# Optimization experiments

Hardware: AMD Instinct MI355X
Metric: run time of the kernel (lower is better)

Reference implementation:

```python
import jax, jax.numpy as jnp
import numpy as np

B = 8192       # batch (tokens)
D = 2048       # data_dim
DEPTH = 3      # tree depth: 1 root + 2 mid + 4 leaf experts
INIT = 0.02


def setup_inputs() -> dict:
    key = jax.random.key(0)
    ks = jax.random.split(key, 6)
    x = jax.random.normal(ks[0], (B, D), dtype=jnp.float32)
    # router output simulated as i.i.d. path bits (router is a frozen pretrained black box)
    path_mask = jax.random.randint(ks[1], (B, DEPTH), 0, 2, dtype=jnp.int32)
    W0 = jax.random.normal(ks[2], (D, D), dtype=jnp.float32) * INIT
    b0 = jnp.zeros((D,), dtype=jnp.float32)
    W1 = jax.random.normal(ks[3], (2, D, D), dtype=jnp.float32) * INIT  # depth-1 experts
    b1 = jnp.zeros((2, D), dtype=jnp.float32)
    W2 = jax.random.normal(ks[4], (4, D, D), dtype=jnp.float32) * INIT  # depth-2 (leaf) experts
    b2 = jnp.zeros((4, D), dtype=jnp.float32)
    return {"x": x, "W0": W0, "b0": b0, "W1": W1, "b1": b1,
            "W2": W2, "b2": b2, "path_mask": path_mask}


def reference(x, W0, b0, W1, b1, W2, b2, path_mask):
    # Root expert (depth 0): applied to all tokens.
    h0 = jax.nn.relu(x @ W0 + b0)                                  # [B, D]
    bit0 = path_mask[:, 0]                                          # routes depth-1 children
    bit1 = path_mask[:, 1]                                          # routes depth-2 children
    # Depth-1: 2 experts; dense compute then per-token select (static-shape MoE dispatch).
    h1_all = jax.nn.relu(jnp.einsum('bd,edf->bef', h0, W1) + b1)    # [B, 2, D]
    h1 = jnp.take_along_axis(h1_all, bit0[:, None, None].astype(jnp.int32), axis=1)[:, 0]
    # Depth-2 (leaves): 4 experts indexed by the 2-bit path.
    leaf = 2 * bit0 + bit1                                          # [B] in {0,1,2,3}
    h2_all = jax.nn.relu(jnp.einsum('bd,edf->bef', h1, W2) + b2)    # [B, 4, D]
    y = jnp.take_along_axis(h2_all, leaf[:, None, None].astype(jnp.int32), axis=1)[:, 0]
    return y
```

## Files before the change

### kernel.cpp

```cpp
#include <hip/hip_runtime.h>

#define BB 8192
#define DD 2048
#define NSLOT 7
#define NP1 (BB + 2*256)
#define NP2 (BB + 4*256)

typedef unsigned short u16;
typedef unsigned int   u32;
typedef unsigned long long u64;

typedef __bf16 bf16x8 __attribute__((ext_vector_type(8)));
typedef float  f32x4  __attribute__((ext_vector_type(4)));
typedef u16    u16x8  __attribute__((ext_vector_type(8)));

#define OFF_WT   0ull
#define OFF_XB   (OFF_WT + (size_t)NSLOT*DD*DD*2)
#define OFF_H0   (OFF_XB + (size_t)BB*DD*2)
#define OFF_P1   (OFF_H0 + (size_t)BB*DD*2)
#define OFF_P2   (OFF_P1 + (size_t)NP1*4)
#define OFF_META (OFF_P2 + (size_t)NP2*4)

__device__ __forceinline__ u16 f2bf(float f) {
  u32 u = __float_as_uint(f);
  u32 r = (u + 0x7FFFu + ((u >> 16) & 1u)) >> 16;
  return (u16)r;
}
__device__ __forceinline__ float bf2f(u16 u) {
  return __uint_as_float(((u32)u) << 16);
}

__device__ __forceinline__ void gld16(const void* g, void* l) {
  __builtin_amdgcn_global_load_lds(
      (const __attribute__((address_space(1))) void*)g,
      (__attribute__((address_space(3))) void*)l, 16, 0, 0);
}


__global__ void k_detect(const u16* x, int* meta) {
  __shared__ int cnt, cntz;
  if (threadIdx.x == 0) { cnt = 0; cntz = 0; }
  __syncthreads();
  u16 u = x[threadIdx.x * 17];
  int ex = (u >> 7) & 0xFF;
  int sane = (ex == 0) || (ex >= 112 && ex <= 143);
  atomicAdd(&cnt, sane);
  atomicAdd(&cntz, (u == 0) ? 1 : 0);
  __syncthreads();
  if (threadIdx.x == 0) meta[20] = (cnt >= 205 && cntz < 64) ? 1 : 0;
}

__global__ __launch_bounds__(1024) void k_route(const int* __restrict__ pm,
                                                int* __restrict__ p1,
                                                int* __restrict__ p2,
                                                int* __restrict__ meta) {
  __shared__ int cnt[6];
  __shared__ int cur[6];
  __shared__ int base1[2], base2[4];
  const int tid = threadIdx.x;
  const int lane = tid & 63;
  if (tid < 6) { cnt[tid] = 0; cur[tid] = 0; }
  __syncthreads();

  for (int i = tid; i < NP1; i += 1024) p1[i] = -1;
  for (int i = tid; i < NP2; i += 1024) p2[i] = -1;

  int myb0[8], myleaf[8];
  #pragma unroll
  for (int i = 0; i < 8; ++i) {
    int b = i * 1024 + tid;
    int b0 = pm[b*3] & 1, b1 = pm[b*3+1] & 1;
    myb0[i] = b0; myleaf[i] = b0*2 + b1;
  }
  #pragma unroll
  for (int i = 0; i < 8; ++i) {
    u64 m0 = __ballot(myb0[i] == 0);
    if (lane == 0) {
      atomicAdd(&cnt[0], __popcll(m0));
      atomicAdd(&cnt[1], 64 - __popcll(m0));
    }
    #pragma unroll
    for (int e = 0; e < 4; ++e) {
      u64 me = __ballot(myleaf[i] == e);
      if (lane == 0) atomicAdd(&cnt[2+e], __popcll(me));
    }
  }
  __syncthreads();
  if (tid == 0) {
    base1[0] = 0;
    base1[1] = (cnt[0] + 255) & ~255;
    meta[12] = 0; meta[13] = base1[1];
    meta[14] = base1[1] + ((cnt[1] + 255) & ~255);
    int b = 0;
    #pragma unroll
    for (int e = 0; e < 4; ++e) {
      base2[e] = b; meta[15+e] = b;
      b += (cnt[2+e] + 255) & ~255;
    }
    meta[19] = b;
  }
  __syncthreads();
  #pragma unroll
  for (int i = 0; i < 8; ++i) {
    int b = i * 1024 + tid;
    u64 lt = (1ull << lane) - 1ull;
    #pragma unroll
    for (int g = 0; g < 2; ++g) {
      u64 m = __ballot(myb0[i] == g);
      int pos = __popcll(m & lt);
      int wbase = 0;
      if (lane == 0 && m) wbase = atomicAdd(&cur[g], __popcll(m));
      wbase = __shfl(wbase, 0);
      if (myb0[i] == g) p1[base1[g] + wbase + pos] = b;
    }
    #pragma unroll
    for (int g = 0; g < 4; ++g) {
      u64 m = __ballot(myleaf[i] == g);
      int pos = __popcll(m & lt);
      int wbase = 0;
      if (lane == 0 && m) wbase = atomicAdd(&cur[2+g], __popcll(m));
      wbase = __shfl(wbase, 0);
      if (myleaf[i] == g) p2[base2[g] + wbase + pos] = b;
    }
  }
}

__global__ void k_cvtx(const void* __restrict__ x, u16* __restrict__ xb,
                       const int* __restrict__ meta) {
  int i = blockIdx.x * 256 + threadIdx.x;
  if (meta[20]) {
    ((uint4*)xb)[i] = ((const uint4*)x)[i];
  } else {
    const float4* p = (const float4*)x + (size_t)i * 2;
    float4 a = p[0], b = p[1];
    uint4 o;
    o.x = f2bf(a.x) | ((u32)f2bf(a.y) << 16);
    o.y = f2bf(a.z) | ((u32)f2bf(a.w) << 16);
    o.z = f2bf(b.x) | ((u32)f2bf(b.y) << 16);
    o.w = f2bf(b.z) | ((u32)f2bf(b.w) << 16);
    ((uint4*)xb)[i] = o;
  }
}

__global__ void k_wt(const void* __restrict__ W0, const void* __restrict__ W1,
                     const void* __restrict__ W2, u16* __restrict__ wt,
                     const int* __restrict__ meta) {
  __shared__ u16 tile[64][66];
  int bid = blockIdx.x;
  int slot = bid >> 10;
  int t = bid & 1023;
  int tr = t >> 5, tc = t & 31;
  const void* src; size_t eoff;
  if (slot == 0)      { src = W0; eoff = 0; }
  else if (slot <= 2) { src = W1; eoff = (size_t)(slot-1)*DD*DD; }
  else                { src = W2; eoff = (size_t)(slot-3)*DD*DD; }
  int r0 = tr*64, c0 = tc*64;
  int tid = threadIdx.x;
  int isbf = meta[20];
  #pragma unroll
  for (int i = 0; i < 4; ++i) {
    int idx = tid + i*256;
    int r = idx >> 4, c4 = (idx & 15) * 4;
    size_t goff = eoff + (size_t)(r0 + r)*DD + c0 + c4;
    u16 v0, v1, v2, v3;
    if (isbf) {
      ushort4 v = *(const ushort4*)((const u16*)src + goff);
      v0 = v.x; v1 = v.y; v2 = v.z; v3 = v.w;
    } else {
      float4 v = *(const float4*)((const float*)src + goff);
      v0 = f2bf(v.x); v1 = f2bf(v.y); v2 = f2bf(v.z); v3 = f2bf(v.w);
    }
    tile[r][c4+0] = v0; tile[r][c4+1] = v1;
    tile[r][c4+2] = v2; tile[r][c4+3] = v3;
  }
  __syncthreads();
  u16* dst = wt + (size_t)slot*DD*DD;
  #pragma unroll
  for (int i = 0; i < 2; ++i) {
    int idx = tid + i*256;
    int n = idx >> 3, j = idx & 7;
    u16x8 o;
    #pragma unroll
    for (int k = 0; k < 8; ++k) o[k] = tile[j*8 + k][n];
    *(u16x8*)&dst[(size_t)(c0 + n)*DD + r0 + j*8] = o;
  }
}

#define SBA(T) ((u32)(((T) & 3) * 24576))
#define SBB(T) ((u32)(((T) & 3) * 24576 + 16384))

#define TILE(T, STAGE, VMN) do {                                             \
  asm volatile("s_waitcnt vmcnt(" #VMN ")" ::: "memory");                    \
  __builtin_amdgcn_s_barrier();                                              \
  {                                                                          \
    if (STAGE) {                                                             \
      const int t3 = (T) + 3;                                                \
      gld16(gA0 + (size_t)t3 * 32, sm + SBA(t3) + wid * 1024);               \
      gld16(gA1 + (size_t)t3 * 32, sm + SBA(t3) + 8192 + wid * 1024);        \
      gld16(gB0 + (size_t)t3 * 32, sm + SBB(t3) + wid * 1024);               \
    }                                                                        \
    const u32 sa = SBA(T) + aoff;                                            \
    const u32 sb = SBB(T) + boff;                                            \
    bf16x8 af[4], bfr[4];                                                    \
    _Pragma("unroll") for (int mt = 0; mt < 4; ++mt)                         \
      af[mt] = *(const bf16x8*)(sm + sa + mt * 1024);                        \
    _Pragma("unroll") for (int nt = 0; nt < 4; ++nt)                         \
      bfr[nt] = *(const bf16x8*)(sm + sb + nt * 1024);                       \
    asm volatile("s_waitcnt lgkmcnt(0)" ::: "memory");                       \
    __builtin_amdgcn_sched_barrier(0);                                       \
    __builtin_amdgcn_s_setprio(1);                                           \
    _Pragma("unroll") for (int mt = 0; mt < 4; ++mt)                         \
      _Pragma("unroll") for (int nt = 0; nt < 4; ++nt)                       \
        acc[mt][nt] = __builtin_amdgcn_mfma_f32_16x16x32_bf16(               \
            af[mt], bfr[nt], acc[mt][nt], 0, 0, 0);                          \
    __builtin_amdgcn_s_setprio(0);                                           \
    __builtin_amdgcn_s_barrier();                                            \
  }                                                                          \
} while (0)

__global__ __launch_bounds__(512, 2) void k_gemm(
    const u16* __restrict__ A, const u16* __restrict__ Wt,
    const void* __restrict__ bias, const int* __restrict__ perm,
    const int* __restrict__ bases, int nexp,
    void* __restrict__ Out, int final_out, const int* __restrict__ meta) {
  __shared__ __align__(16) char sm[4 * 24576];

  const int tid  = threadIdx.x;
  const int wid  = tid >> 6;
  const int lane = tid & 63;

  const u32 nwg = gridDim.x * gridDim.y;
  const u32 wg  = blockIdx.y * gridDim.x + blockIdx.x;
  const u32 cpx = nwg >> 3;
  const u32 swz = (wg & 7u) * cpx + (wg >> 3);
  const int m0 = (int)(swz >> 4) * 256;
  const int n0 = (int)(swz & 15u) * 128;

  int e = 0;
  if (nexp == 2)      e = (m0 >= bases[1]);
  else if (nexp == 4) e = (m0 >= bases[1]) + (m0 >= bases[2]) + (m0 >= bases[3]);
  if (perm && m0 >= bases[nexp]) return;
  const u16* W = Wt + (size_t)e * DD * DD;

  const int sr = wid * 16 + (lane >> 2);
  const int kc = (lane & 3) * 8;
  int ar0 = m0 + sr, ar1 = m0 + 128 + sr;
  if (perm) {
    int v0 = perm[ar0]; ar0 = v0 < 0 ? 0 : v0;
    int v1 = perm[ar1]; ar1 = v1 < 0 ? 0 : v1;
  }
  const u16* gA0 = A + (size_t)ar0 * DD + kc;
  const u16* gA1 = A + (size_t)ar1 * DD + kc;
  const u16* gB0 = W + (size_t)(n0 + sr) * DD + kc;

  const int wm = wid >> 1, wn = wid & 1;
  const int q = lane >> 4, cl = lane & 15;
  const u32 aoff = (u32)((wm * 64 + cl) * 64 + q * 16);
  const u32 boff = (u32)((wn * 64 + cl) * 64 + q * 16);

  f32x4 zero = {0.0f, 0.0f, 0.0f, 0.0f};
  f32x4 acc[4][4];
  #pragma unroll
  for (int i = 0; i < 4; ++i)
    #pragma unroll
    for (int j = 0; j < 4; ++j) acc[i][j] = zero;

  #pragma unroll
  for (int tt = 0; tt < 3; ++tt) {
    gld16(gA0 + (size_t)tt * 32, sm + SBA(tt) + wid * 1024);
    gld16(gA1 + (size_t)tt * 32, sm + SBA(tt) + 8192 + wid * 1024);
    gld16(gB0 + (size_t)tt * 32, sm + SBB(tt) + wid * 1024);
  }

  #pragma unroll 1
  for (int t = 0; t < 61; ++t) TILE(t, true, 6);
  TILE(61, false, 6);
  TILE(62, false, 3);
  TILE(63, false, 0);

  const int isbf = meta[20];
  float bv[4];
  #pragma unroll
  for (int nt = 0; nt < 4; ++nt) {
    int col = n0 + wn * 64 + nt * 16 + cl;
    bv[nt] = isbf ? bf2f(((const u16*)bias)[e * DD + col])
                  : ((const float*)bias)[e * DD + col];
  }
  #pragma unroll
  for (int mt = 0; mt < 4; ++mt) {
    int rbase = m0 + wm * 64 + mt * 16 + q * 4;
    #pragma unroll
    for (int r = 0; r < 4; ++r) {
      int row = rbase + r;
      int orow = row;
      if (perm) { orow = perm[row]; if (orow < 0) continue; }
      #pragma unroll
      for (int nt = 0; nt < 4; ++nt) {
        int col = n0 + wn * 64 + nt * 16 + cl;
        float v = acc[mt][nt][r] + bv[nt];
        v = v > 0.0f ? v : 0.0f;
        if (!final_out || isbf) ((u16*)Out)[(size_t)orow * DD + col] = f2bf(v);
        else                    ((float*)Out)[(size_t)orow * DD + col] = v;
      }
    }
  }
}

#undef TILE
#undef SBA
#undef SBB

extern "C" void kernel_launch(void* const* d_in, const int* in_sizes, int n_in,
                              void* d_out, int out_size, void* d_ws, size_t ws_size,
                              hipStream_t stream) {
  (void)in_sizes; (void)n_in; (void)out_size; (void)ws_size;
  const void* x  = d_in[0];
  const void* W0 = d_in[1];
  const void* b0 = d_in[2];
  const void* W1 = d_in[3];
  const void* b1 = d_in[4];
  const void* W2 = d_in[5];
  const void* b2 = d_in[6];
  const int*  pm = (const int*)d_in[7];

  char* ws  = (char*)d_ws;
  u16*  wt  = (u16*)(ws + OFF_WT);
  u16*  xb  = (u16*)(ws + OFF_XB);
  u16*  h0  = (u16*)(ws + OFF_H0);
  u16*  h1  = xb;
  int*  p1  = (int*)(ws + OFF_P1);
  int*  p2  = (int*)(ws + OFF_P2);
  int*  meta= (int*)(ws + OFF_META);

  hipLaunchKernelGGL(k_detect, dim3(1),  dim3(256),  0, stream, (const u16*)x, meta);
  hipLaunchKernelGGL(k_route,  dim3(1),  dim3(1024), 0, stream, pm, p1, p2, meta);
  hipLaunchKernelGGL(k_cvtx,   dim3(BB*DD/8/256), dim3(256), 0, stream, x, xb, meta);
  hipLaunchKernelGGL(k_wt,     dim3(7*1024), dim3(256), 0, stream, W0, W1, W2, wt, meta);

  hipLaunchKernelGGL(k_gemm, dim3(16, 32), dim3(512), 0, stream,
                     xb, wt, b0, (const int*)nullptr, (const int*)nullptr, 1,
                     (void*)h0, 0, meta);
  hipLaunchKernelGGL(k_gemm, dim3(16, NP1/256), dim3(512), 0, stream,
                     h0, wt + (size_t)1*DD*DD, b1, p1, meta + 12, 2,
                     (void*)h1, 0, meta);
  hipLaunchKernelGGL(k_gemm, dim3(16, NP2/256), dim3(512), 0, stream,
                     h1, wt + (size_t)3*DD*DD, b2, p2, meta + 15, 4,
                     d_out, 1, meta);
}
```

Before: 558.2 us.

## Use 4-wave blocks with 128x64 warp tiles, 3-stage LDS pipeline, swizzled LDS

Cuts the GEMM block from 8 waves to 4 waves. Each wave now computes a 128x64 sub-tile with 32 accumulators, which raises register-level reuse of the A and B fragments. The LDS ring drops from 4 to 3 buffers, prefetching 2 tiles ahead, and uses an XOR swizzle on the k-chunk to avoid bank conflicts. The trade-off is higher register pressure per wave and less latency hiding, since there are fewer waves and a shallower prefetch.

```diff
diff --git a/kernel.cpp b/kernel.cpp
--- a/kernel.cpp
+++ b/kernel.cpp
@@ -186,30 +186,32 @@
   }
 }
 
-#define SBA(T) ((u32)(((T) & 3) * 24576))
-#define SBB(T) ((u32)(((T) & 3) * 24576 + 16384))
-
-#define TILE(T, STAGE, VMN) do {                                             \
+#define STG(SBUF, TI) do {                                                   \
+    const size_t ko = (size_t)(TI) * 32;                                     \
+    gld16(gA0 + ko, sm + (SBUF)*24576 +         0 + widoff);                 \
+    gld16(gA1 + ko, sm + (SBUF)*24576 +      4096 + widoff);                 \
+    gld16(gA2 + ko, sm + (SBUF)*24576 +      8192 + widoff);                 \
+    gld16(gA3 + ko, sm + (SBUF)*24576 +     12288 + widoff);                 \
+    gld16(gB0 + ko, sm + (SBUF)*24576 + 16384 + 0 + widoff);                 \
+    gld16(gB1 + ko, sm + (SBUF)*24576 + 16384 + 4096 + widoff);              \
+  } while (0)
+
+#define TILE(BUF, T, STAGE, SBUF, VMN) do {                                  \
   asm volatile("s_waitcnt vmcnt(" #VMN ")" ::: "memory");                    \
   __builtin_amdgcn_s_barrier();                                              \
   {                                                                          \
-    if (STAGE) {                                                             \
-      const int t3 = (T) + 3;                                                \
-      gld16(gA0 + (size_t)t3 * 32, sm + SBA(t3) + wid * 1024);               \
-      gld16(gA1 + (size_t)t3 * 32, sm + SBA(t3) + 8192 + wid * 1024);        \
-      gld16(gB0 + (size_t)t3 * 32, sm + SBB(t3) + wid * 1024);               \
-    }                                                                        \
-    const u32 sa = SBA(T) + aoff;                                            \
-    const u32 sb = SBB(T) + boff;                                            \
-    bf16x8 af[4], bfr[4];                                                    \
-    _Pragma("unroll") for (int mt = 0; mt < 4; ++mt)                         \
+    if (STAGE) STG(SBUF, (T) + 2);                                           \
+    const u32 sa = (BUF)*24576 + aoff;                                       \
+    const u32 sb = (BUF)*24576 + 16384 + boff;                               \
+    bf16x8 af[8], bfr[4];                                                    \
+    _Pragma("unroll") for (int mt = 0; mt < 8; ++mt)                         \
       af[mt] = *(const bf16x8*)(sm + sa + mt * 1024);                        \
     _Pragma("unroll") for (int nt = 0; nt < 4; ++nt)                         \
       bfr[nt] = *(const bf16x8*)(sm + sb + nt * 1024);                       \
     asm volatile("s_waitcnt lgkmcnt(0)" ::: "memory");                       \
     __builtin_amdgcn_sched_barrier(0);                                       \
     __builtin_amdgcn_s_setprio(1);                                           \
-    _Pragma("unroll") for (int mt = 0; mt < 4; ++mt)                         \
+    _Pragma("unroll") for (int mt = 0; mt < 8; ++mt)                         \
       _Pragma("unroll") for (int nt = 0; nt < 4; ++nt)                       \
         acc[mt][nt] = __builtin_amdgcn_mfma_f32_16x16x32_bf16(               \
             af[mt], bfr[nt], acc[mt][nt], 0, 0, 0);                          \
@@ -218,16 +220,17 @@
   }                                                                          \
 } while (0)
 
-__global__ __launch_bounds__(512, 2) void k_gemm(
+__global__ __launch_bounds__(256, 2) void k_gemm(
     const u16* __restrict__ A, const u16* __restrict__ Wt,
     const void* __restrict__ bias, const int* __restrict__ perm,
     const int* __restrict__ bases, int nexp,
     void* __restrict__ Out, int final_out, const int* __restrict__ meta) {
-  __shared__ __align__(16) char sm[4 * 24576];
+  __shared__ __align__(16) char sm[3 * 24576];
 
   const int tid  = threadIdx.x;
   const int wid  = tid >> 6;
   const int lane = tid & 63;
+  const u32 widoff = (u32)wid * 1024;
 
   const u32 nwg = gridDim.x * gridDim.y;
   const u32 wg  = blockIdx.y * gridDim.x + blockIdx.x;
@@ -242,41 +245,48 @@
   if (perm && m0 >= bases[nexp]) return;
   const u16* W = Wt + (size_t)e * DD * DD;
 
-  const int sr = wid * 16 + (lane >> 2);
-  const int kc = (lane & 3) * 8;
-  int ar0 = m0 + sr, ar1 = m0 + 128 + sr;
-  if (perm) {
-    int v0 = perm[ar0]; ar0 = v0 < 0 ? 0 : v0;
-    int v1 = perm[ar1]; ar1 = v1 < 0 ? 0 : v1;
-  }
-  const u16* gA0 = A + (size_t)ar0 * DD + kc;
-  const u16* gA1 = A + (size_t)ar1 * DD + kc;
+  const int sr = tid >> 2;
+  const int kc = ((tid & 3) ^ ((tid >> 3) & 3)) * 8;
+  int ar[4];
+  #pragma unroll
+  for (int j = 0; j < 4; ++j) {
+    int r = m0 + j * 64 + sr;
+    if (perm) { int v = perm[r]; r = (v < 0) ? 0 : v; }
+    ar[j] = r;
+  }
+  const u16* gA0 = A + (size_t)ar[0] * DD + kc;
+  const u16* gA1 = A + (size_t)ar[1] * DD + kc;
+  const u16* gA2 = A + (size_t)ar[2] * DD + kc;
+  const u16* gA3 = A + (size_t)ar[3] * DD + kc;
   const u16* gB0 = W + (size_t)(n0 + sr) * DD + kc;
+  const u16* gB1 = W + (size_t)(n0 + 64 + sr) * DD + kc;
 
   const int wm = wid >> 1, wn = wid & 1;
   const int q = lane >> 4, cl = lane & 15;
-  const u32 aoff = (u32)((wm * 64 + cl) * 64 + q * 16);
-  const u32 boff = (u32)((wn * 64 + cl) * 64 + q * 16);
+  const int sw = q ^ ((cl >> 1) & 3);
+  const u32 aoff = (u32)((wm * 128 + cl) * 64 + sw * 16);
+  const u32 boff = (u32)((wn * 64 + cl) * 64 + sw * 16);
 
   f32x4 zero = {0.0f, 0.0f, 0.0f, 0.0f};
-  f32x4 acc[4][4];
-  #pragma unroll
-  for (int i = 0; i < 4; ++i)
+  f32x4 acc[8][4];
+  #pragma unroll
+  for (int i = 0; i < 8; ++i)
     #pragma unroll
     for (int j = 0; j < 4; ++j) acc[i][j] = zero;
 
-  #pragma unroll
-  for (int tt = 0; tt < 3; ++tt) {
-    gld16(gA0 + (size_t)tt * 32, sm + SBA(tt) + wid * 1024);
-    gld16(gA1 + (size_t)tt * 32, sm + SBA(tt) + 8192 + wid * 1024);
-    gld16(gB0 + (size_t)tt * 32, sm + SBB(tt) + wid * 1024);
-  }
+  STG(0, 0);
+  STG(1, 1);
 
   #pragma unroll 1
-  for (int t = 0; t < 61; ++t) TILE(t, true, 6);
-  TILE(61, false, 6);
-  TILE(62, false, 3);
-  TILE(63, false, 0);
+  for (int t = 0; t < 60; t += 3) {
+    TILE(0, t + 0, 1, 2, 6);
+    TILE(1, t + 1, 1, 0, 6);
+    TILE(2, t + 2, 1, 1, 6);
+  }
+  TILE(0, 60, 1, 2, 6);
+  TILE(1, 61, 1, 0, 6);
+  TILE(2, 62, 0, 0, 6);
+  TILE(0, 63, 0, 0, 0);
 
   const int isbf = meta[20];
   float bv[4];
@@ -287,8 +297,8 @@
                   : ((const float*)bias)[e * DD + col];
   }
   #pragma unroll
-  for (int mt = 0; mt < 4; ++mt) {
-    int rbase = m0 + wm * 64 + mt * 16 + q * 4;
+  for (int mt = 0; mt < 8; ++mt) {
+    int rbase = m0 + wm * 128 + mt * 16 + q * 4;
     #pragma unroll
     for (int r = 0; r < 4; ++r) {
       int row = rbase + r;
@@ -307,8 +317,7 @@
 }
 
 #undef TILE
-#undef SBA
-#undef SBB
+#undef STG
 
 extern "C" void kernel_launch(void* const* d_in, const int* in_sizes, int n_in,
                               void* d_out, int out_size, void* d_ws, size_t ws_size,
@@ -337,13 +346,13 @@
   hipLaunchKernelGGL(k_cvtx,   dim3(BB*DD/8/256), dim3(256), 0, stream, x, xb, meta);
   hipLaunchKernelGGL(k_wt,     dim3(7*1024), dim3(256), 0, stream, W0, W1, W2, wt, meta);
 
-  hipLaunchKernelGGL(k_gemm, dim3(16, 32), dim3(512), 0, stream,
+  hipLaunchKernelGGL(k_gemm, dim3(16, 32), dim3(256), 0, stream,
                      xb, wt, b0, (const int*)nullptr, (const int*)nullptr, 1,
                      (void*)h0, 0, meta);
-  hipLaunchKernelGGL(k_gemm, dim3(16, NP1/256), dim3(512), 0, stream,
+  hipLaunchKernelGGL(k_gemm, dim3(16, NP1/256), dim3(256), 0, stream,
                      h0, wt + (size_t)1*DD*DD, b1, p1, meta + 12, 2,
                      (void*)h1, 0, meta);
-  hipLaunchKernelGGL(k_gemm, dim3(16, NP2/256), dim3(512), 0, stream,
+  hipLaunchKernelGGL(k_gemm, dim3(16, NP2/256), dim3(256), 0, stream,
                      h1, wt + (size_t)3*DD*DD, b2, p2, meta + 15, 4,
                      d_out, 1, meta);
 }
```

After: 522.5 us. -6.4%, faster.

## Restage GEMM mainloop with 64-wide K tiles, swizzled LDS and split half-stages

Applied to the files above, without the earlier changes.

The bf16 GEMM main loop now works on 64-wide K tiles. Each tile is split into two half-stages whose global-to-LDS loads are issued between the MFMA batches. The buffer ring grows to six 24KB LDS slots allocated dynamically. An XOR swizzle on the K-chunk column is meant to cut LDS bank conflicts, and the trailing per-tile barrier is removed. The goal is to hide more load latency and lower synchronisation cost per unit of K. In exchange, the roughly 147KB of LDS allows only one workgroup per CU, contrary to the launch-bounds hint, and relies on the device allowing that much dynamic LDS.

```diff
diff --git a/kernel.cpp b/kernel.cpp
--- a/kernel.cpp
+++ b/kernel.cpp
@@ -186,35 +186,47 @@
   }
 }
 
-#define SBA(T) ((u32)(((T) & 3) * 24576))
-#define SBB(T) ((u32)(((T) & 3) * 24576 + 16384))
-
-#define TILE(T, STAGE, VMN) do {                                             \
+#define STGH(SLOT, P, TI) do {                                               \
+    const size_t ko = (size_t)(TI) * 64;                                     \
+    gld16(gA##P##0 + ko, sm + (SLOT)*24576 +     0 + widoff);                \
+    gld16(gA##P##1 + ko, sm + (SLOT)*24576 +  8192 + widoff);                \
+    gld16(gB##P    + ko, sm + (SLOT)*24576 + 16384 + widoff);                \
+  } while (0)
+
+#define TILE(S0, S1, SS0, SS1, T, STAGE, VMN) do {                           \
   asm volatile("s_waitcnt vmcnt(" #VMN ")" ::: "memory");                    \
   __builtin_amdgcn_s_barrier();                                              \
   {                                                                          \
-    if (STAGE) {                                                             \
-      const int t3 = (T) + 3;                                                \
-      gld16(gA0 + (size_t)t3 * 32, sm + SBA(t3) + wid * 1024);               \
-      gld16(gA1 + (size_t)t3 * 32, sm + SBA(t3) + 8192 + wid * 1024);        \
-      gld16(gB0 + (size_t)t3 * 32, sm + SBB(t3) + wid * 1024);               \
-    }                                                                        \
-    const u32 sa = SBA(T) + aoff;                                            \
-    const u32 sb = SBB(T) + boff;                                            \
-    bf16x8 af[4], bfr[4];                                                    \
+    const u32 sA = (ahalf ? (u32)(S1) : (u32)(S0)) * 24576u + arow;          \
+    const u32 sB = (bhalf ? (u32)(S1) : (u32)(S0)) * 24576u + 16384u + brow; \
+    bf16x8 a0[4], b0[4];                                                     \
     _Pragma("unroll") for (int mt = 0; mt < 4; ++mt)                         \
-      af[mt] = *(const bf16x8*)(sm + sa + mt * 1024);                        \
+      a0[mt] = *(const bf16x8*)(sm + sA + mt*2048 + o0);                     \
     _Pragma("unroll") for (int nt = 0; nt < 4; ++nt)                         \
-      bfr[nt] = *(const bf16x8*)(sm + sb + nt * 1024);                       \
+      b0[nt] = *(const bf16x8*)(sm + sB + nt*2048 + o0);                     \
+    if (STAGE) STGH(SS0, 0, (T) + 2);                                        \
     asm volatile("s_waitcnt lgkmcnt(0)" ::: "memory");                       \
     __builtin_amdgcn_sched_barrier(0);                                       \
     __builtin_amdgcn_s_setprio(1);                                           \
     _Pragma("unroll") for (int mt = 0; mt < 4; ++mt)                         \
       _Pragma("unroll") for (int nt = 0; nt < 4; ++nt)                       \
         acc[mt][nt] = __builtin_amdgcn_mfma_f32_16x16x32_bf16(               \
-            af[mt], bfr[nt], acc[mt][nt], 0, 0, 0);                          \
+            a0[mt], b0[nt], acc[mt][nt], 0, 0, 0);                           \
     __builtin_amdgcn_s_setprio(0);                                           \
-    __builtin_amdgcn_s_barrier();                                            \
+    bf16x8 a1[4], b1[4];                                                     \
+    _Pragma("unroll") for (int mt = 0; mt < 4; ++mt)                         \
+      a1[mt] = *(const bf16x8*)(sm + sA + mt*2048 + o1);                     \
+    _Pragma("unroll") for (int nt = 0; nt < 4; ++nt)                         \
+      b1[nt] = *(const bf16x8*)(sm + sB + nt*2048 + o1);                     \
+    if (STAGE) STGH(SS1, 1, (T) + 2);                                        \
+    asm volatile("s_waitcnt lgkmcnt(0)" ::: "memory");                       \
+    __builtin_amdgcn_sched_barrier(0);                                       \
+    __builtin_amdgcn_s_setprio(1);                                           \
+    _Pragma("unroll") for (int mt = 0; mt < 4; ++mt)                         \
+      _Pragma("unroll") for (int nt = 0; nt < 4; ++nt)                       \
+        acc[mt][nt] = __builtin_amdgcn_mfma_f32_16x16x32_bf16(               \
+            a1[mt], b1[nt], acc[mt][nt], 0, 0, 0);                           \
+    __builtin_amdgcn_s_setprio(0);                                           \
   }                                                                          \
 } while (0)
 
@@ -223,11 +235,12 @@
     const void* __restrict__ bias, const int* __restrict__ perm,
     const int* __restrict__ bases, int nexp,
     void* __restrict__ Out, int final_out, const int* __restrict__ meta) {
-  __shared__ __align__(16) char sm[4 * 24576];
+  extern __shared__ __align__(16) char sm[];
 
   const int tid  = threadIdx.x;
   const int wid  = tid >> 6;
   const int lane = tid & 63;
+  const u32 widoff = (u32)wid * 1024;
 
   const u32 nwg = gridDim.x * gridDim.y;
   const u32 wg  = blockIdx.y * gridDim.x + blockIdx.x;
@@ -242,21 +255,32 @@
   if (perm && m0 >= bases[nexp]) return;
   const u16* W = Wt + (size_t)e * DD * DD;
 
-  const int sr = wid * 16 + (lane >> 2);
-  const int kc = (lane & 3) * 8;
-  int ar0 = m0 + sr, ar1 = m0 + 128 + sr;
-  if (perm) {
-    int v0 = perm[ar0]; ar0 = v0 < 0 ? 0 : v0;
-    int v1 = perm[ar1]; ar1 = v1 < 0 ? 0 : v1;
-  }
-  const u16* gA0 = A + (size_t)ar0 * DD + kc;
-  const u16* gA1 = A + (size_t)ar1 * DD + kc;
-  const u16* gB0 = W + (size_t)(n0 + sr) * DD + kc;
+  const int sr = tid >> 3;
+  const int kc = ((tid & 7) ^ (sr & 7)) * 8;
+  int arr[4];
+  #pragma unroll
+  for (int p = 0; p < 2; ++p)
+    #pragma unroll
+    for (int s = 0; s < 2; ++s) {
+      int r = m0 + p * 128 + s * 64 + sr;
+      if (perm) { int v = perm[r]; r = (v < 0) ? 0 : v; }
+      arr[p * 2 + s] = r;
+    }
+  const u16* gA00 = A + (size_t)arr[0] * DD + kc;
+  const u16* gA01 = A + (size_t)arr[1] * DD + kc;
+  const u16* gA10 = A + (size_t)arr[2] * DD + kc;
+  const u16* gA11 = A + (size_t)arr[3] * DD + kc;
+  const u16* gB0  = W + (size_t)(n0 + sr) * DD + kc;
+  const u16* gB1  = W + (size_t)(n0 + 64 + sr) * DD + kc;
 
   const int wm = wid >> 1, wn = wid & 1;
+  const int ahalf = wid >> 2;
+  const int bhalf = wn;
   const int q = lane >> 4, cl = lane & 15;
-  const u32 aoff = (u32)((wm * 64 + cl) * 64 + q * 16);
-  const u32 boff = (u32)((wn * 64 + cl) * 64 + q * 16);
+  const u32 arow = (u32)(((wm & 1) * 64 + cl) * 128);
+  const u32 brow = (u32)(cl * 128);
+  const u32 o0 = (u32)(((cl >> 2) & 1) * 64 + (q ^ (cl & 3)) * 16);
+  const u32 o1 = o0 ^ 64u;
 
   f32x4 zero = {0.0f, 0.0f, 0.0f, 0.0f};
   f32x4 acc[4][4];
@@ -265,18 +289,19 @@
     #pragma unroll
     for (int j = 0; j < 4; ++j) acc[i][j] = zero;
 
-  #pragma unroll
-  for (int tt = 0; tt < 3; ++tt) {
-    gld16(gA0 + (size_t)tt * 32, sm + SBA(tt) + wid * 1024);
-    gld16(gA1 + (size_t)tt * 32, sm + SBA(tt) + 8192 + wid * 1024);
-    gld16(gB0 + (size_t)tt * 32, sm + SBB(tt) + wid * 1024);
-  }
+  STGH(0, 0, 0);
+  STGH(1, 1, 0);
+  STGH(2, 0, 1);
+  STGH(3, 1, 1);
 
   #pragma unroll 1
-  for (int t = 0; t < 61; ++t) TILE(t, true, 6);
-  TILE(61, false, 6);
-  TILE(62, false, 3);
-  TILE(63, false, 0);
+  for (int t = 0; t < 30; t += 3) {
+    TILE(0, 1, 4, 5, t + 0, 1, 6);
+    TILE(2, 3, 0, 1, t + 1, 1, 6);
+    TILE(4, 5, 2, 3, t + 2, 1, 6);
+  }
+  TILE(0, 1, 0, 0, 30, 0, 6);
+  TILE(2, 3, 0, 0, 31, 0, 0);
 
   const int isbf = meta[20];
   float bv[4];
@@ -307,8 +332,7 @@
 }
 
 #undef TILE
-#undef SBA
-#undef SBB
+#undef STGH
 
 extern "C" void kernel_launch(void* const* d_in, const int* in_sizes, int n_in,
                               void* d_out, int out_size, void* d_ws, size_t ws_size,
@@ -332,18 +356,20 @@
   int*  p2  = (int*)(ws + OFF_P2);
   int*  meta= (int*)(ws + OFF_META);
 
+  const size_t LDSB = 6 * 24576;
+
   hipLaunchKernelGGL(k_detect, dim3(1),  dim3(256),  0, stream, (const u16*)x, meta);
   hipLaunchKernelGGL(k_route,  dim3(1),  dim3(1024), 0, stream, pm, p1, p2, meta);
   hipLaunchKernelGGL(k_cvtx,   dim3(BB*DD/8/256), dim3(256), 0, stream, x, xb, meta);
   hipLaunchKernelGGL(k_wt,     dim3(7*1024), dim3(256), 0, stream, W0, W1, W2, wt, meta);
 
-  hipLaunchKernelGGL(k_gemm, dim3(16, 32), dim3(512), 0, stream,
+  hipLaunchKernelGGL(k_gemm, dim3(16, 32), dim3(512), LDSB, stream,
                      xb, wt, b0, (const int*)nullptr, (const int*)nullptr, 1,
                      (void*)h0, 0, meta);
-  hipLaunchKernelGGL(k_gemm, dim3(16, NP1/256), dim3(512), 0, stream,
+  hipLaunchKernelGGL(k_gemm, dim3(16, NP1/256), dim3(512), LDSB, stream,
                      h0, wt + (size_t)1*DD*DD, b1, p1, meta + 12, 2,
                      (void*)h1, 0, meta);
-  hipLaunchKernelGGL(k_gemm, dim3(16, NP2/256), dim3(512), 0, stream,
+  hipLaunchKernelGGL(k_gemm, dim3(16, NP2/256), dim3(512), LDSB, stream,
                      h1, wt + (size_t)3*DD*DD, b2, p2, meta + 15, 4,
                      d_out, 1, meta);
 }
```

Result: faster. 505.1 us (-9.5%).
